# Optimization experiments

Hardware: AMD Instinct MI355X
Metric: run time of the kernel (lower is better)

Reference implementation:

```python
import jax, jax.numpy as jnp
import numpy as np
import math

B, T, C = 2, 2048, 768
NH, HD = 12, 64  # n_head, head_dim

def setup_inputs() -> dict:
    key = jax.random.key(0)
    k1, k2, k3 = jax.random.split(key, 3)
    x = jax.random.normal(k1, (B, T, C), dtype=jnp.float32)
    mask = jnp.tril(jnp.ones((T, T), dtype=bool))[None, None]  # [1,1,T,T] causal
    Wqkv = jax.random.normal(k2, (C, 3 * C), dtype=jnp.float32) * (1.0 / math.sqrt(C))
    Wproj = jax.random.normal(k3, (C, C), dtype=jnp.float32) * (1.0 / math.sqrt(C))
    return {"x": x, "mask": mask, "Wqkv": Wqkv, "Wproj": Wproj}

def reference(x, mask, Wqkv, Wproj):
    b, t, c = x.shape
    qkv = x @ Wqkv  # [b,t,3c]
    q, k, v = jnp.split(qkv, 3, axis=-1)
    q = q.reshape(b, t, NH, HD).transpose(0, 2, 1, 3)  # [b,h,t,d]
    k = k.reshape(b, t, NH, HD).transpose(0, 2, 1, 3)
    v = v.reshape(b, t, NH, HD).transpose(0, 2, 1, 3)
    att = jnp.einsum('bhqd,bhkd->bhqk', q, k) / math.sqrt(HD)
    att = jnp.where(mask, att, -jnp.inf)
    att = jax.nn.softmax(att, axis=-1)
    out = jnp.einsum('bhqk,bhkd->bhqd', att, v)
    out = out.transpose(0, 2, 1, 3).reshape(b, t, c)
    return out @ Wproj
```

## Files before the change

### kernel.cpp

```cpp
#include <hip/hip_runtime.h>
#include <hip/hip_bf16.h>

#define T_   2048
#define C_   768
#define NH_  12
#define HD_  64
#define M_   (2*T_)
#define N1_  (3*C_)
#define PB_  ((size_t)NH_*T_*HD_)
#define KS_  0.180336880f
#define MK_  8.65617024f

typedef __attribute__((ext_vector_type(8))) short  short8;
typedef __attribute__((ext_vector_type(4))) short  shortx4;
typedef __attribute__((ext_vector_type(4))) float  floatx4;

__device__ __forceinline__ floatx4 mfma_bf16(short8 a, short8 b, floatx4 c) {
    return __builtin_amdgcn_mfma_f32_16x16x32_bf16(a, b, c, 0, 0, 0);
}
__device__ __forceinline__ float fast_exp2(float x) {
    return __builtin_amdgcn_exp2f(x);
}
__device__ __forceinline__ void lds_fence() {
    asm volatile("s_waitcnt lgkmcnt(0)" ::: "memory");
}
__device__ __forceinline__ void async_load16(const __hip_bfloat16* g, __hip_bfloat16* l) {
    __builtin_amdgcn_global_load_lds(
        (const __attribute__((address_space(1))) void*)g,
        (__attribute__((address_space(3))) void*)l, 16, 0, 0);
}

__global__ __launch_bounds__(256) void prep_all(const float* __restrict__ x,
                                                const float* __restrict__ wqkv,
                                                const float* __restrict__ wproj,
                                                __hip_bfloat16* __restrict__ xb,
                                                __hip_bfloat16* __restrict__ wqkvT,
                                                __hip_bfloat16* __restrict__ wprojT) {
    if (blockIdx.x < 3072) {
        const int idx = blockIdx.x * 256 + threadIdx.x;
        const floatx4 v = ((const floatx4*)x)[idx];
        union { __hip_bfloat16 h[4]; shortx4 s; } u;
#pragma unroll
        for (int j = 0; j < 4; j++) u.h[j] = __float2bfloat16(v[j]);
        ((shortx4*)xb)[idx] = u.s;
    } else if (blockIdx.x < 3936) {
        const int j  = (blockIdx.x - 3072) * 256 + threadIdx.x;
        const int k8 = j / N1_;
        const int n  = j - k8 * N1_;
        union { __hip_bfloat16 h[8]; short8 s; } u;
#pragma unroll
        for (int jj = 0; jj < 8; jj++)
            u.h[jj] = __float2bfloat16(wqkv[(size_t)(k8 * 8 + jj) * N1_ + n]);
        *(short8*)(wqkvT + (size_t)n * C_ + k8 * 8) = u.s;
    } else {
        const int j  = (blockIdx.x - 3936) * 256 + threadIdx.x;
        const int k8 = j / C_;
        const int n  = j - k8 * C_;
        union { __hip_bfloat16 h[8]; short8 s; } u;
#pragma unroll
        for (int jj = 0; jj < 8; jj++)
            u.h[jj] = __float2bfloat16(wproj[(size_t)(k8 * 8 + jj) * C_ + n]);
        *(short8*)(wprojT + (size_t)n * C_ + k8 * 8) = u.s;
    }
}

__global__ __launch_bounds__(256) void prep1(const float* __restrict__ x,
                                             const float* __restrict__ wqkv,
                                             __hip_bfloat16* __restrict__ xb,
                                             __hip_bfloat16* __restrict__ wqkvT) {
    if (blockIdx.x < 3072) {
        const int idx = blockIdx.x * 256 + threadIdx.x;
        const floatx4 v = ((const floatx4*)x)[idx];
        union { __hip_bfloat16 h[4]; shortx4 s; } u;
#pragma unroll
        for (int j = 0; j < 4; j++) u.h[j] = __float2bfloat16(v[j]);
        ((shortx4*)xb)[idx] = u.s;
    } else {
        const int j  = (blockIdx.x - 3072) * 256 + threadIdx.x;
        const int k8 = j / N1_;
        const int n  = j - k8 * N1_;
        union { __hip_bfloat16 h[8]; short8 s; } u;
#pragma unroll
        for (int jj = 0; jj < 8; jj++)
            u.h[jj] = __float2bfloat16(wqkv[(size_t)(k8 * 8 + jj) * N1_ + n]);
        *(short8*)(wqkvT + (size_t)n * C_ + k8 * 8) = u.s;
    }
}
__global__ __launch_bounds__(256) void prep2(const float* __restrict__ wproj,
                                             __hip_bfloat16* __restrict__ wprojT) {
    const int j  = blockIdx.x * 256 + threadIdx.x;
    const int k8 = j / C_;
    const int n  = j - k8 * C_;
    union { __hip_bfloat16 h[8]; short8 s; } u;
#pragma unroll
    for (int jj = 0; jj < 8; jj++)
        u.h[jj] = __float2bfloat16(wproj[(size_t)(k8 * 8 + jj) * C_ + n]);
    *(short8*)(wprojT + (size_t)n * C_ + k8 * 8) = u.s;
}

__global__ __launch_bounds__(256) void gemm_bt64x128(const __hip_bfloat16* __restrict__ A,
                                                     const __hip_bfloat16* __restrict__ Bt,
                                                     int N, int K,
                                                     __hip_bfloat16* __restrict__ O0,
                                                     __hip_bfloat16* __restrict__ O1,
                                                     __hip_bfloat16* __restrict__ O2) {
    __shared__ __align__(16) __hip_bfloat16 As[2 * 64 * 32];
    __shared__ __align__(16) __hip_bfloat16 Bs[2 * 128 * 32];

    const int tid  = threadIdx.x;
    const int n0   = blockIdx.x * 128;
    const int m0   = blockIdx.y * 64;
    const int wave = tid >> 6;
    const int ln   = tid & 63;
    const int l16  = ln & 15;
    const int q4   = ln >> 4;
    const int wm   = (wave >> 1) * 32;
    const int wn   = (wave & 1) * 64;

    const int lrow = ln >> 2;
    const int loct = (ln & 3) * 8;
    const __hip_bfloat16* ApD  = A  + (size_t)(m0 + wave * 16 + lrow) * K + loct;
    const __hip_bfloat16* BpD0 = Bt + (size_t)(n0 + (2 * wave)     * 16 + lrow) * K + loct;
    const __hip_bfloat16* BpD1 = Bt + (size_t)(n0 + (2 * wave + 1) * 16 + lrow) * K + loct;

    floatx4 acc[2][4];
#pragma unroll
    for (int i = 0; i < 2; i++)
#pragma unroll
        for (int j = 0; j < 4; j++) acc[i][j] = (floatx4){0.f, 0.f, 0.f, 0.f};

    async_load16(ApD,  As + wave * 512);
    async_load16(BpD0, Bs + (2 * wave) * 512);
    async_load16(BpD1, Bs + (2 * wave + 1) * 512);
    __syncthreads();

    const int NT = K >> 5;
    int cur = 0;
    for (int t = 0; t < NT; ++t) {
        if (t < NT - 1) {
            const int k1 = (t + 1) * 32;
            const int alt = (cur ^ 1);
            async_load16(ApD  + k1, As + alt * 2048 + wave * 512);
            async_load16(BpD0 + k1, Bs + alt * 4096 + (2 * wave) * 512);
            async_load16(BpD1 + k1, Bs + alt * 4096 + (2 * wave + 1) * 512);
        }
        const __hip_bfloat16* Asc = As + cur * 2048;
        const __hip_bfloat16* Bsc = Bs + cur * 4096;
        short8 af[2], bfr[4];
#pragma unroll
        for (int i = 0; i < 2; i++)
            af[i] = *(const short8*)(Asc + (wm + i * 16 + l16) * 32 + q4 * 8);
#pragma unroll
        for (int j = 0; j < 4; j++)
            bfr[j] = *(const short8*)(Bsc + (wn + j * 16 + l16) * 32 + q4 * 8);
#pragma unroll
        for (int i = 0; i < 2; i++)
#pragma unroll
            for (int j = 0; j < 4; j++)
                acc[i][j] = mfma_bf16(af[i], bfr[j], acc[i][j]);
        __syncthreads();
        cur ^= 1;
    }

#pragma unroll
    for (int i = 0; i < 2; i++) {
        const int mbase = m0 + wm + i * 16 + q4 * 4;
#pragma unroll
        for (int j = 0; j < 4; j++) {
            const int n = n0 + wn + j * 16 + l16;
            const int which = n / C_;
            const int rem   = n - which * C_;
            const int h     = rem >> 6;
            const int d     = rem & 63;
#pragma unroll
            for (int r = 0; r < 4; r++) {
                const int mm = mbase + r;
                const __hip_bfloat16 hv = __float2bfloat16(acc[i][j][r]);
                const int bh = (mm >> 11) * NH_ + h;
                const int t  = mm & (T_ - 1);
                if (which == 0)      O0[((size_t)bh * T_ + t) * HD_ + d] = hv;
                else if (which == 1) O1[((size_t)bh * T_ + t) * HD_ + d] = hv;
                else                 O2[((size_t)bh * HD_ + d) * T_ + t] = hv;
            }
        }
    }
}

__global__ __launch_bounds__(256) void gemm_bt64(const __hip_bfloat16* __restrict__ A,
                                                 const __hip_bfloat16* __restrict__ Bt,
                                                 int N, int K,
                                                 float* __restrict__ O0) {
    __shared__ __align__(16) __hip_bfloat16 As[64 * 40];
    __shared__ __align__(16) __hip_bfloat16 Bs[64 * 40];

    const int tid  = threadIdx.x;
    const int n0   = blockIdx.x * 64;
    const int m0   = blockIdx.y * 64;
    const int srow = tid >> 2;
    const int scol = (tid & 3) * 8;
    const int wave = tid >> 6;
    const int ln   = tid & 63;
    const int l16  = ln & 15;
    const int q4   = ln >> 4;
    const int wm   = (wave >> 1) * 32;
    const int wn   = (wave & 1) * 32;

    floatx4 acc[2][2];
#pragma unroll
    for (int i = 0; i < 2; i++)
#pragma unroll
        for (int j = 0; j < 2; j++) acc[i][j] = (floatx4){0.f, 0.f, 0.f, 0.f};

    const __hip_bfloat16* Ap = A  + (size_t)(m0 + srow) * K + scol;
    const __hip_bfloat16* Bp = Bt + (size_t)(n0 + srow) * K + scol;

    for (int k0 = 0; k0 < K; k0 += 32) {
        short8 av = *(const short8*)(Ap + k0);
        short8 bv = *(const short8*)(Bp + k0);
        __syncthreads();
        *(short8*)(As + srow * 40 + scol) = av;
        *(short8*)(Bs + srow * 40 + scol) = bv;
        __syncthreads();
        short8 af[2], bfr[2];
#pragma unroll
        for (int i = 0; i < 2; i++) {
            af[i]  = *(const short8*)(As + (wm + i * 16 + l16) * 40 + q4 * 8);
            bfr[i] = *(const short8*)(Bs + (wn + i * 16 + l16) * 40 + q4 * 8);
        }
#pragma unroll
        for (int i = 0; i < 2; i++)
#pragma unroll
            for (int j = 0; j < 2; j++)
                acc[i][j] = mfma_bf16(af[i], bfr[j], acc[i][j]);
    }

#pragma unroll
    for (int i = 0; i < 2; i++) {
        const int mbase = m0 + wm + i * 16 + q4 * 4;
#pragma unroll
        for (int j = 0; j < 2; j++) {
            const int n = n0 + wn + j * 16 + l16;
#pragma unroll
            for (int r = 0; r < 4; r++)
                O0[(size_t)(mbase + r) * N + n] = acc[i][j][r];
        }
    }
}

__global__ __launch_bounds__(256) void attn_fused(const __hip_bfloat16* __restrict__ Q,
                                                  const __hip_bfloat16* __restrict__ Kd,
                                                  const __hip_bfloat16* __restrict__ Vt,
                                                  __hip_bfloat16* __restrict__ O) {
    __shared__ __align__(16) __hip_bfloat16 plds[4][2][16][72];

    const int bh   = blockIdx.x;
    const int wid  = threadIdx.x >> 6;
    const int lane = threadIdx.x & 63;
    const int l16  = lane & 15;
    const int q4   = lane >> 4;
    const int i    = 63 - (int)blockIdx.y;
    const int q0A  = 32 * i;
    const int q0B  = 32 * i + 16;
    const int nch  = (i >> 1) + 1;

    const __hip_bfloat16* Qh = Q  + (size_t)bh * T_ * HD_;
    const __hip_bfloat16* Kh = Kd + (size_t)bh * T_ * HD_;
    const __hip_bfloat16* Vh = Vt + (size_t)bh * HD_ * T_;

    short8 aqA[2], aqB[2];
#pragma unroll
    for (int kt = 0; kt < 2; kt++) {
        aqA[kt] = *(const short8*)(Qh + (size_t)(q0A + l16) * HD_ + kt * 32 + q4 * 8);
        aqB[kt] = *(const short8*)(Qh + (size_t)(q0B + l16) * HD_ + kt * 32 + q4 * 8);
    }

    floatx4 accA[4], accB[4];
#pragma unroll
    for (int ct = 0; ct < 4; ct++) {
        accA[ct] = (floatx4){0.f, 0.f, 0.f, 0.f};
        accB[ct] = (floatx4){0.f, 0.f, 0.f, 0.f};
    }
    float sumA = 0.f, sumB = 0.f;

    for (int c = wid; c < nch; c += 4) {
        const int kv0 = c * 64;
        const bool diag = (c == nch - 1);

        short8 bk[4][2];
#pragma unroll
        for (int nt = 0; nt < 4; nt++)
#pragma unroll
            for (int kt = 0; kt < 2; kt++)
                bk[nt][kt] = *(const short8*)(Kh + (size_t)(kv0 + nt * 16 + l16) * HD_ + kt * 32 + q4 * 8);

        short8 bv[4][2];
#pragma unroll
        for (int ct = 0; ct < 4; ct++)
#pragma unroll
            for (int kt = 0; kt < 2; kt++)
                bv[ct][kt] = *(const short8*)(Vh + (size_t)(ct * 16 + l16) * T_ + kv0 + kt * 32 + q4 * 8);

        floatx4 sA[4], sB[4];
#pragma unroll
        for (int nt = 0; nt < 4; nt++) {
            sA[nt] = (floatx4){0.f, 0.f, 0.f, 0.f};
            sB[nt] = (floatx4){0.f, 0.f, 0.f, 0.f};
#pragma unroll
            for (int kt = 0; kt < 2; kt++) {
                sA[nt] = mfma_bf16(bk[nt][kt], aqA[kt], sA[nt]);
                sB[nt] = mfma_bf16(bk[nt][kt], aqB[kt], sB[nt]);
            }
        }

        if (diag) {
#pragma unroll
            for (int nt = 0; nt < 4; nt++) {
#pragma unroll
                for (int r = 0; r < 4; r++) {
                    const int kvg = kv0 + nt * 16 + q4 * 4 + r;
                    if (kvg > q0A + l16) sA[nt][r] = -3e38f;
                    if (kvg > q0B + l16) sB[nt][r] = -3e38f;
                }
            }
        }

#pragma unroll
        for (int nt = 0; nt < 4; nt++) {
            union { __hip_bfloat16 h[4]; shortx4 s; } uA, uB;
            float pA[4], pB[4];
#pragma unroll
            for (int r = 0; r < 4; r++) {
                pA[r] = fast_exp2(sA[nt][r] * KS_ - MK_);
                pB[r] = fast_exp2(sB[nt][r] * KS_ - MK_);
                uA.h[r] = __float2bfloat16(pA[r]);
                uB.h[r] = __float2bfloat16(pB[r]);
            }
            sumA += (pA[0] + pA[1]) + (pA[2] + pA[3]);
            sumB += (pB[0] + pB[1]) + (pB[2] + pB[3]);
            *(shortx4*)(&plds[wid][0][l16][nt * 16 + q4 * 4]) = uA.s;
            *(shortx4*)(&plds[wid][1][l16][nt * 16 + q4 * 4]) = uB.s;
        }

        lds_fence();

        short8 apA[2], apB[2];
#pragma unroll
        for (int kt = 0; kt < 2; kt++) {
            apA[kt] = *(const short8*)(&plds[wid][0][l16][kt * 32 + q4 * 8]);
            apB[kt] = *(const short8*)(&plds[wid][1][l16][kt * 32 + q4 * 8]);
        }
#pragma unroll
        for (int ct = 0; ct < 4; ct++)
#pragma unroll
            for (int kt = 0; kt < 2; kt++) {
                accA[ct] = mfma_bf16(apA[kt], bv[ct][kt], accA[ct]);
                accB[ct] = mfma_bf16(apB[kt], bv[ct][kt], accB[ct]);
            }

        lds_fence();
    }

    sumA += __shfl_xor(sumA, 16, 64);
    sumA += __shfl_xor(sumA, 32, 64);
    sumB += __shfl_xor(sumB, 16, 64);
    sumB += __shfl_xor(sumB, 32, 64);

    __syncthreads();
    floatx4* accbuf = (floatx4*)&plds[0][0][0][0];
    float*   lbuf   = (float*)((char*)&plds[0][0][0][0] + 16384);

    auto publish = [&](int slot) {
#pragma unroll
        for (int ct = 0; ct < 4; ct++) {
            accbuf[((slot * 2 + 0) * 4 + ct) * 64 + lane] = accA[ct];
            accbuf[((slot * 2 + 1) * 4 + ct) * 64 + lane] = accB[ct];
        }
        if (q4 == 0) {
            lbuf[(slot * 2 + 0) * 16 + l16] = sumA;
            lbuf[(slot * 2 + 1) * 16 + l16] = sumB;
        }
    };
    auto mergeIn = [&](int slot) {
#pragma unroll
        for (int ct = 0; ct < 4; ct++) {
            accA[ct] += accbuf[((slot * 2 + 0) * 4 + ct) * 64 + lane];
            accB[ct] += accbuf[((slot * 2 + 1) * 4 + ct) * 64 + lane];
        }
        sumA += lbuf[(slot * 2 + 0) * 16 + l16];
        sumB += lbuf[(slot * 2 + 1) * 16 + l16];
    };

    if (wid >= 2) publish(wid - 2);
    __syncthreads();
    if (wid < 2) mergeIn(wid);
    __syncthreads();
    if (wid == 1) publish(0);
    __syncthreads();
    if (wid == 0) {
        mergeIn(0);
        const int orow0 = (bh / NH_) * T_;
        const int hcol  = (bh % NH_) * HD_;
#pragma unroll
        for (int r = 0; r < 4; r++) {
            const float invA = 1.0f / __shfl(sumA, q4 * 4 + r, 64);
            const float invB = 1.0f / __shfl(sumB, q4 * 4 + r, 64);
            __hip_bfloat16* oA = O + (size_t)(orow0 + q0A + q4 * 4 + r) * C_ + hcol;
            __hip_bfloat16* oB = O + (size_t)(orow0 + q0B + q4 * 4 + r) * C_ + hcol;
#pragma unroll
            for (int ct = 0; ct < 4; ct++) {
                oA[ct * 16 + l16] = __float2bfloat16(accA[ct][r] * invA);
                oB[ct * 16 + l16] = __float2bfloat16(accB[ct][r] * invB);
            }
        }
    }
}

extern "C" void kernel_launch(void* const* d_in, const int* in_sizes, int n_in,
                              void* d_out, int out_size, void* d_ws, size_t ws_size,
                              hipStream_t stream) {
    const float *x = nullptr, *wqkv = nullptr, *wproj = nullptr;
    for (int i = 0; i < n_in; i++) {
        const int s = in_sizes[i];
        if (s == M_ * C_ && !x) x = (const float*)d_in[i];
        else if (s == C_ * N1_ && !wqkv) wqkv = (const float*)d_in[i];
        else if (s == C_ * C_ && !wproj) wproj = (const float*)d_in[i];
    }
    float* out = (float*)d_out;
    __hip_bfloat16* ws = (__hip_bfloat16*)d_ws;
    __hip_bfloat16* Vt = (__hip_bfloat16*)d_out;

    __hip_bfloat16* Qall  = ws;
    __hip_bfloat16* Kall  = Qall + 2 * PB_;
    __hip_bfloat16* ATT   = Kall + 2 * PB_;
    __hip_bfloat16* xb    = ATT;
    __hip_bfloat16* wqkvT = (__hip_bfloat16*)d_out + 2 * PB_;

    const size_t needMerged = (6 * PB_ + (size_t)C_ * C_) * sizeof(__hip_bfloat16);
    if (ws_size >= needMerged) {
        __hip_bfloat16* wprojT = ws + 6 * PB_;
        prep_all<<<dim3(4224), 256, 0, stream>>>(x, wqkv, wproj, xb, wqkvT, wprojT);
        gemm_bt64x128<<<dim3(N1_ / 128, M_ / 64), 256, 0, stream>>>(
            xb, wqkvT, N1_, C_, Qall, Kall, Vt);
        attn_fused<<<dim3(2 * NH_, 64), 256, 0, stream>>>(Qall, Kall, Vt, ATT);
        gemm_bt64<<<dim3(C_ / 64, M_ / 64), 256, 0, stream>>>(ATT, wprojT, C_, C_, out);
    } else {
        __hip_bfloat16* wprojT = Qall;
        prep1<<<dim3(3936), 256, 0, stream>>>(x, wqkv, xb, wqkvT);
        gemm_bt64x128<<<dim3(N1_ / 128, M_ / 64), 256, 0, stream>>>(
            xb, wqkvT, N1_, C_, Qall, Kall, Vt);
        attn_fused<<<dim3(2 * NH_, 64), 256, 0, stream>>>(Qall, Kall, Vt, ATT);
        prep2<<<dim3(288), 256, 0, stream>>>(wproj, wprojT);
        gemm_bt64<<<dim3(C_ / 64, M_ / 64), 256, 0, stream>>>(ATT, wprojT, C_, C_, out);
    }
}
```

Measured before the change: 194.4 us.

## Fuse pipeline stages into one persistent kernel with grid-wide barriers

```diff
diff --git a/kernel.cpp b/kernel.cpp
--- a/kernel.cpp
+++ b/kernel.cpp
@@ -10,6 +10,7 @@
 #define PB_  ((size_t)NH_*T_*HD_)
 #define KS_  0.180336880f
 #define MK_  8.65617024f
+#define NBLK 768
 
 typedef __attribute__((ext_vector_type(8))) short  short8;
 typedef __attribute__((ext_vector_type(4))) short  shortx4;
@@ -30,106 +31,86 @@
         (__attribute__((address_space(3))) void*)l, 16, 0, 0);
 }
 
-__global__ __launch_bounds__(256) void prep_all(const float* __restrict__ x,
-                                                const float* __restrict__ wqkv,
-                                                const float* __restrict__ wproj,
-                                                __hip_bfloat16* __restrict__ xb,
-                                                __hip_bfloat16* __restrict__ wqkvT,
-                                                __hip_bfloat16* __restrict__ wprojT) {
-    if (blockIdx.x < 3072) {
-        const int idx = blockIdx.x * 256 + threadIdx.x;
+__device__ __forceinline__ void grid_sync(unsigned int* cnt, unsigned int target) {
+    __builtin_amdgcn_fence(__ATOMIC_RELEASE, "agent");
+    __syncthreads();
+    if (threadIdx.x == 0) {
+        __hip_atomic_fetch_add(cnt, 1u, __ATOMIC_RELAXED, __HIP_MEMORY_SCOPE_AGENT);
+        while (__hip_atomic_load(cnt, __ATOMIC_RELAXED, __HIP_MEMORY_SCOPE_AGENT) < target)
+            __builtin_amdgcn_s_sleep(2);
+    }
+    __syncthreads();
+    __builtin_amdgcn_fence(__ATOMIC_ACQUIRE, "agent");
+}
+
+
+__device__ __forceinline__ void prep_unit(unsigned u, const float* __restrict__ x,
+                                          const float* __restrict__ wqkv,
+                                          const float* __restrict__ wproj,
+                                          __hip_bfloat16* __restrict__ xb,
+                                          __hip_bfloat16* __restrict__ wqkvT,
+                                          __hip_bfloat16* __restrict__ wprojT) {
+    if (u < 3072u) {
+        const int idx = u * 256 + threadIdx.x;
         const floatx4 v = ((const floatx4*)x)[idx];
-        union { __hip_bfloat16 h[4]; shortx4 s; } u;
-#pragma unroll
-        for (int j = 0; j < 4; j++) u.h[j] = __float2bfloat16(v[j]);
-        ((shortx4*)xb)[idx] = u.s;
-    } else if (blockIdx.x < 3936) {
-        const int j  = (blockIdx.x - 3072) * 256 + threadIdx.x;
+        union { __hip_bfloat16 h[4]; shortx4 s; } w;
+#pragma unroll
+        for (int j = 0; j < 4; j++) w.h[j] = __float2bfloat16(v[j]);
+        ((shortx4*)xb)[idx] = w.s;
+    } else if (u < 3936u) {
+        const int j  = (u - 3072) * 256 + threadIdx.x;
         const int k8 = j / N1_;
         const int n  = j - k8 * N1_;
-        union { __hip_bfloat16 h[8]; short8 s; } u;
+        union { __hip_bfloat16 h[8]; short8 s; } w;
 #pragma unroll
         for (int jj = 0; jj < 8; jj++)
-            u.h[jj] = __float2bfloat16(wqkv[(size_t)(k8 * 8 + jj) * N1_ + n]);
-        *(short8*)(wqkvT + (size_t)n * C_ + k8 * 8) = u.s;
+            w.h[jj] = __float2bfloat16(wqkv[(size_t)(k8 * 8 + jj) * N1_ + n]);
+        *(short8*)(wqkvT + (size_t)n * C_ + k8 * 8) = w.s;
     } else {
-        const int j  = (blockIdx.x - 3936) * 256 + threadIdx.x;
+        const int j  = (u - 3936) * 256 + threadIdx.x;
         const int k8 = j / C_;
         const int n  = j - k8 * C_;
-        union { __hip_bfloat16 h[8]; short8 s; } u;
+        union { __hip_bfloat16 h[8]; short8 s; } w;
 #pragma unroll
         for (int jj = 0; jj < 8; jj++)
-            u.h[jj] = __float2bfloat16(wproj[(size_t)(k8 * 8 + jj) * C_ + n]);
-        *(short8*)(wprojT + (size_t)n * C_ + k8 * 8) = u.s;
-    }
-}
-
-__global__ __launch_bounds__(256) void prep1(const float* __restrict__ x,
-                                             const float* __restrict__ wqkv,
-                                             __hip_bfloat16* __restrict__ xb,
-                                             __hip_bfloat16* __restrict__ wqkvT) {
-    if (blockIdx.x < 3072) {
-        const int idx = blockIdx.x * 256 + threadIdx.x;
-        const floatx4 v = ((const floatx4*)x)[idx];
-        union { __hip_bfloat16 h[4]; shortx4 s; } u;
-#pragma unroll
-        for (int j = 0; j < 4; j++) u.h[j] = __float2bfloat16(v[j]);
-        ((shortx4*)xb)[idx] = u.s;
-    } else {
-        const int j  = (blockIdx.x - 3072) * 256 + threadIdx.x;
-        const int k8 = j / N1_;
-        const int n  = j - k8 * N1_;
-        union { __hip_bfloat16 h[8]; short8 s; } u;
-#pragma unroll
-        for (int jj = 0; jj < 8; jj++)
-            u.h[jj] = __float2bfloat16(wqkv[(size_t)(k8 * 8 + jj) * N1_ + n]);
-        *(short8*)(wqkvT + (size_t)n * C_ + k8 * 8) = u.s;
-    }
-}
-__global__ __launch_bounds__(256) void prep2(const float* __restrict__ wproj,
-                                             __hip_bfloat16* __restrict__ wprojT) {
-    const int j  = blockIdx.x * 256 + threadIdx.x;
-    const int k8 = j / C_;
-    const int n  = j - k8 * C_;
-    union { __hip_bfloat16 h[8]; short8 s; } u;
-#pragma unroll
-    for (int jj = 0; jj < 8; jj++)
-        u.h[jj] = __float2bfloat16(wproj[(size_t)(k8 * 8 + jj) * C_ + n]);
-    *(short8*)(wprojT + (size_t)n * C_ + k8 * 8) = u.s;
-}
-
-__global__ __launch_bounds__(256) void gemm_bt64x128(const __hip_bfloat16* __restrict__ A,
-                                                     const __hip_bfloat16* __restrict__ Bt,
-                                                     int N, int K,
-                                                     __hip_bfloat16* __restrict__ O0,
-                                                     __hip_bfloat16* __restrict__ O1,
-                                                     __hip_bfloat16* __restrict__ O2) {
-    __shared__ __align__(16) __hip_bfloat16 As[2 * 64 * 32];
-    __shared__ __align__(16) __hip_bfloat16 Bs[2 * 128 * 32];
-
+            w.h[jj] = __float2bfloat16(wproj[(size_t)(k8 * 8 + jj) * C_ + n]);
+        *(short8*)(wprojT + (size_t)n * C_ + k8 * 8) = w.s;
+    }
+}
+
+__device__ __forceinline__ void gemm128_block(int bx, int by,
+                                              const __hip_bfloat16* __restrict__ A,
+                                              const __hip_bfloat16* __restrict__ Bt,
+                                              int N, int K,
+                                              __hip_bfloat16* __restrict__ O0,
+                                              __hip_bfloat16* __restrict__ O1,
+                                              __hip_bfloat16* __restrict__ O2,
+                                              __hip_bfloat16* As, __hip_bfloat16* Bs) {
     const int tid  = threadIdx.x;
-    const int n0   = blockIdx.x * 128;
-    const int m0   = blockIdx.y * 64;
+    const int n0   = bx * 128;
+    const int m0   = by * 128;
     const int wave = tid >> 6;
     const int ln   = tid & 63;
     const int l16  = ln & 15;
     const int q4   = ln >> 4;
-    const int wm   = (wave >> 1) * 32;
+    const int wm   = (wave >> 1) * 64;
     const int wn   = (wave & 1) * 64;
 
     const int lrow = ln >> 2;
     const int loct = (ln & 3) * 8;
-    const __hip_bfloat16* ApD  = A  + (size_t)(m0 + wave * 16 + lrow) * K + loct;
+    const __hip_bfloat16* ApD0 = A  + (size_t)(m0 + (2 * wave)     * 16 + lrow) * K + loct;
+    const __hip_bfloat16* ApD1 = A  + (size_t)(m0 + (2 * wave + 1) * 16 + lrow) * K + loct;
     const __hip_bfloat16* BpD0 = Bt + (size_t)(n0 + (2 * wave)     * 16 + lrow) * K + loct;
     const __hip_bfloat16* BpD1 = Bt + (size_t)(n0 + (2 * wave + 1) * 16 + lrow) * K + loct;
 
-    floatx4 acc[2][4];
-#pragma unroll
-    for (int i = 0; i < 2; i++)
+    floatx4 acc[4][4];
+#pragma unroll
+    for (int i = 0; i < 4; i++)
 #pragma unroll
         for (int j = 0; j < 4; j++) acc[i][j] = (floatx4){0.f, 0.f, 0.f, 0.f};
 
-    async_load16(ApD,  As + wave * 512);
+    async_load16(ApD0, As + (2 * wave) * 512);
+    async_load16(ApD1, As + (2 * wave + 1) * 512);
     async_load16(BpD0, Bs + (2 * wave) * 512);
     async_load16(BpD1, Bs + (2 * wave + 1) * 512);
     __syncthreads();
@@ -138,23 +119,24 @@
     int cur = 0;
     for (int t = 0; t < NT; ++t) {
         if (t < NT - 1) {
-            const int k1 = (t + 1) * 32;
-            const int alt = (cur ^ 1);
-            async_load16(ApD  + k1, As + alt * 2048 + wave * 512);
+            const int k1  = (t + 1) * 32;
+            const int alt = cur ^ 1;
+            async_load16(ApD0 + k1, As + alt * 4096 + (2 * wave) * 512);
+            async_load16(ApD1 + k1, As + alt * 4096 + (2 * wave + 1) * 512);
             async_load16(BpD0 + k1, Bs + alt * 4096 + (2 * wave) * 512);
             async_load16(BpD1 + k1, Bs + alt * 4096 + (2 * wave + 1) * 512);
         }
-        const __hip_bfloat16* Asc = As + cur * 2048;
+        const __hip_bfloat16* Asc = As + cur * 4096;
         const __hip_bfloat16* Bsc = Bs + cur * 4096;
-        short8 af[2], bfr[4];
-#pragma unroll
-        for (int i = 0; i < 2; i++)
+        short8 af[4], bfr[4];
+#pragma unroll
+        for (int i = 0; i < 4; i++)
             af[i] = *(const short8*)(Asc + (wm + i * 16 + l16) * 32 + q4 * 8);
 #pragma unroll
         for (int j = 0; j < 4; j++)
             bfr[j] = *(const short8*)(Bsc + (wn + j * 16 + l16) * 32 + q4 * 8);
 #pragma unroll
-        for (int i = 0; i < 2; i++)
+        for (int i = 0; i < 4; i++)
 #pragma unroll
             for (int j = 0; j < 4; j++)
                 acc[i][j] = mfma_bf16(af[i], bfr[j], acc[i][j]);
@@ -163,7 +145,7 @@
     }
 
 #pragma unroll
-    for (int i = 0; i < 2; i++) {
+    for (int i = 0; i < 4; i++) {
         const int mbase = m0 + wm + i * 16 + q4 * 4;
 #pragma unroll
         for (int j = 0; j < 4; j++) {
@@ -186,16 +168,15 @@
     }
 }
 
-__global__ __launch_bounds__(256) void gemm_bt64(const __hip_bfloat16* __restrict__ A,
-                                                 const __hip_bfloat16* __restrict__ Bt,
-                                                 int N, int K,
-                                                 float* __restrict__ O0) {
-    __shared__ __align__(16) __hip_bfloat16 As[64 * 40];
-    __shared__ __align__(16) __hip_bfloat16 Bs[64 * 40];
-
+__device__ __forceinline__ void gemm64_block(int bx, int by,
+                                             const __hip_bfloat16* __restrict__ A,
+                                             const __hip_bfloat16* __restrict__ Bt,
+                                             int N, int K,
+                                             float* __restrict__ O0,
+                                             __hip_bfloat16* As, __hip_bfloat16* Bs) {
     const int tid  = threadIdx.x;
-    const int n0   = blockIdx.x * 64;
-    const int m0   = blockIdx.y * 64;
+    const int n0   = bx * 64;
+    const int m0   = by * 64;
     const int srow = tid >> 2;
     const int scol = (tid & 3) * 8;
     const int wave = tid >> 6;
@@ -247,18 +228,17 @@
     }
 }
 
-__global__ __launch_bounds__(256) void attn_fused(const __hip_bfloat16* __restrict__ Q,
-                                                  const __hip_bfloat16* __restrict__ Kd,
-                                                  const __hip_bfloat16* __restrict__ Vt,
-                                                  __hip_bfloat16* __restrict__ O) {
-    __shared__ __align__(16) __hip_bfloat16 plds[4][2][16][72];
-
-    const int bh   = blockIdx.x;
+typedef __hip_bfloat16 plds_t[2][16][72];
+__device__ __forceinline__ void attn_block(int bh, int i,
+                                           const __hip_bfloat16* __restrict__ Q,
+                                           const __hip_bfloat16* __restrict__ Kd,
+                                           const __hip_bfloat16* __restrict__ Vt,
+                                           __hip_bfloat16* __restrict__ O,
+                                           plds_t* plds) {
     const int wid  = threadIdx.x >> 6;
     const int lane = threadIdx.x & 63;
     const int l16  = lane & 15;
     const int q4   = lane >> 4;
-    const int i    = 63 - (int)blockIdx.y;
     const int q0A  = 32 * i;
     const int q0B  = 32 * i + 16;
     const int nch  = (i >> 1) + 1;
@@ -413,6 +393,104 @@
             }
         }
     }
+    __syncthreads();
+}
+
+__global__ __launch_bounds__(256, 4) void mega(const float* __restrict__ x,
+                                               const float* __restrict__ wqkv,
+                                               const float* __restrict__ wproj,
+                                               __hip_bfloat16* __restrict__ xb,
+                                               __hip_bfloat16* __restrict__ wqkvT,
+                                               __hip_bfloat16* __restrict__ wprojT,
+                                               __hip_bfloat16* __restrict__ Qall,
+                                               __hip_bfloat16* __restrict__ Kall,
+                                               __hip_bfloat16* __restrict__ Vt,
+                                               __hip_bfloat16* __restrict__ ATT,
+                                               float* __restrict__ out,
+                                               unsigned int* cnt) {
+    __shared__ __align__(16) char arena[32768];
+
+    for (unsigned u = blockIdx.x; u < 4224u; u += NBLK)
+        prep_unit(u, x, wqkv, wproj, xb, wqkvT, wprojT);
+    grid_sync(cnt, 1u * NBLK);
+
+    if (blockIdx.x < 576u) {
+        gemm128_block((int)(blockIdx.x % 18u), (int)(blockIdx.x / 18u),
+                      xb, wqkvT, N1_, C_, Qall, Kall, Vt,
+                      (__hip_bfloat16*)arena, (__hip_bfloat16*)(arena + 16384));
+    }
+    grid_sync(cnt, 2u * NBLK);
+
+    {
+        plds_t* plds = (plds_t*)arena;
+        const unsigned u1 = blockIdx.x, u2 = 1535u - blockIdx.x;
+        attn_block((int)(u1 % 24u), 63 - (int)(u1 / 24u), Qall, Kall, Vt, ATT, plds);
+        attn_block((int)(u2 % 24u), 63 - (int)(u2 / 24u), Qall, Kall, Vt, ATT, plds);
+    }
+    grid_sync(cnt, 3u * NBLK);
+
+    gemm64_block((int)(blockIdx.x % 12u), (int)(blockIdx.x / 12u),
+                 ATT, wprojT, C_, C_, out,
+                 (__hip_bfloat16*)arena, (__hip_bfloat16*)(arena + 5120));
+}
+
+__global__ __launch_bounds__(256) void prep1(const float* __restrict__ x,
+                                             const float* __restrict__ wqkv,
+                                             __hip_bfloat16* __restrict__ xb,
+                                             __hip_bfloat16* __restrict__ wqkvT) {
+    if (blockIdx.x < 3072) {
+        const int idx = blockIdx.x * 256 + threadIdx.x;
+        const floatx4 v = ((const floatx4*)x)[idx];
+        union { __hip_bfloat16 h[4]; shortx4 s; } u;
+#pragma unroll
+        for (int j = 0; j < 4; j++) u.h[j] = __float2bfloat16(v[j]);
+        ((shortx4*)xb)[idx] = u.s;
+    } else {
+        const int j  = (blockIdx.x - 3072) * 256 + threadIdx.x;
+        const int k8 = j / N1_;
+        const int n  = j - k8 * N1_;
+        union { __hip_bfloat16 h[8]; short8 s; } u;
+#pragma unroll
+        for (int jj = 0; jj < 8; jj++)
+            u.h[jj] = __float2bfloat16(wqkv[(size_t)(k8 * 8 + jj) * N1_ + n]);
+        *(short8*)(wqkvT + (size_t)n * C_ + k8 * 8) = u.s;
+    }
+}
+__global__ __launch_bounds__(256) void prep2(const float* __restrict__ wproj,
+                                             __hip_bfloat16* __restrict__ wprojT) {
+    const int j  = blockIdx.x * 256 + threadIdx.x;
+    const int k8 = j / C_;
+    const int n  = j - k8 * C_;
+    union { __hip_bfloat16 h[8]; short8 s; } u;
+#pragma unroll
+    for (int jj = 0; jj < 8; jj++)
+        u.h[jj] = __float2bfloat16(wproj[(size_t)(k8 * 8 + jj) * C_ + n]);
+    *(short8*)(wprojT + (size_t)n * C_ + k8 * 8) = u.s;
+}
+__global__ __launch_bounds__(256) void gemm_bt128(const __hip_bfloat16* __restrict__ A,
+                                                  const __hip_bfloat16* __restrict__ Bt,
+                                                  int N, int K,
+                                                  __hip_bfloat16* __restrict__ O0,
+                                                  __hip_bfloat16* __restrict__ O1,
+                                                  __hip_bfloat16* __restrict__ O2) {
+    __shared__ __align__(16) char ar[32768];
+    gemm128_block(blockIdx.x, blockIdx.y, A, Bt, N, K, O0, O1, O2,
+                  (__hip_bfloat16*)ar, (__hip_bfloat16*)(ar + 16384));
+}
+__global__ __launch_bounds__(256) void gemm_bt64(const __hip_bfloat16* __restrict__ A,
+                                                 const __hip_bfloat16* __restrict__ Bt,
+                                                 int N, int K,
+                                                 float* __restrict__ O0) {
+    __shared__ __align__(16) char ar[10240];
+    gemm64_block(blockIdx.x, blockIdx.y, A, Bt, N, K, O0,
+                 (__hip_bfloat16*)ar, (__hip_bfloat16*)(ar + 5120));
+}
+__global__ __launch_bounds__(256) void attn_fused(const __hip_bfloat16* __restrict__ Q,
+                                                  const __hip_bfloat16* __restrict__ Kd,
+                                                  const __hip_bfloat16* __restrict__ Vt,
+                                                  __hip_bfloat16* __restrict__ O) {
+    __shared__ __align__(16) char ar[18432];
+    attn_block(blockIdx.x, 63 - (int)blockIdx.y, Q, Kd, Vt, O, (plds_t*)ar);
 }
 
 extern "C" void kernel_launch(void* const* d_in, const int* in_sizes, int n_in,
@@ -438,15 +516,14 @@
     const size_t needMerged = (6 * PB_ + (size_t)C_ * C_) * sizeof(__hip_bfloat16);
     if (ws_size >= needMerged) {
         __hip_bfloat16* wprojT = ws + 6 * PB_;
-        prep_all<<<dim3(4224), 256, 0, stream>>>(x, wqkv, wproj, xb, wqkvT, wprojT);
-        gemm_bt64x128<<<dim3(N1_ / 128, M_ / 64), 256, 0, stream>>>(
-            xb, wqkvT, N1_, C_, Qall, Kall, Vt);
-        attn_fused<<<dim3(2 * NH_, 64), 256, 0, stream>>>(Qall, Kall, Vt, ATT);
-        gemm_bt64<<<dim3(C_ / 64, M_ / 64), 256, 0, stream>>>(ATT, wprojT, C_, C_, out);
+        unsigned int* cnt = (unsigned int*)((char*)d_out + (size_t)M_ * C_ * 4 - 64);
+        (void)hipMemsetAsync(cnt, 0, 64, stream);
+        mega<<<dim3(NBLK), 256, 0, stream>>>(x, wqkv, wproj, xb, wqkvT, wprojT,
+                                             Qall, Kall, Vt, ATT, out, cnt);
     } else {
         __hip_bfloat16* wprojT = Qall;
         prep1<<<dim3(3936), 256, 0, stream>>>(x, wqkv, xb, wqkvT);
-        gemm_bt64x128<<<dim3(N1_ / 128, M_ / 64), 256, 0, stream>>>(
+        gemm_bt128<<<dim3(N1_ / 128, M_ / 128), 256, 0, stream>>>(
             xb, wqkvT, N1_, C_, Qall, Kall, Vt);
         attn_fused<<<dim3(2 * NH_, 64), 256, 0, stream>>>(Qall, Kall, Vt, ATT);
         prep2<<<dim3(288), 256, 0, stream>>>(wproj, wprojT);
```

Result: slower. 625.2 us (+221.5%).
